# Optimization experiments

Measured on AMD Instinct MI355X. Metric: run time of the kernel, lower is better.

Reference implementation:

```python
import jax, jax.numpy as jnp
import numpy as np

LN_EPS = 1e-5


def setup_inputs() -> dict:
    key = jax.random.key(0)
    ks = jax.random.split(key, 4)
    N, D, E, Hd = 65536, 256, 8, 1024  # nodes, dim, n_experts, hidden_dim=4*dim
    s = 0.02
    return {
        "H": jax.random.normal(ks[0], (N, D), dtype=jnp.float32),
        "gate_w": jax.random.normal(ks[1], (D, E), dtype=jnp.float32) * s,
        "gate_b": jnp.zeros((E,), jnp.float32),
        "W1": jax.random.normal(ks[2], (E, D, Hd), dtype=jnp.float32) * s,
        "b1": jnp.zeros((E, Hd), jnp.float32),
        "W2": jax.random.normal(ks[3], (E, Hd, D), dtype=jnp.float32) * s,
        "b2": jnp.zeros((E, D), jnp.float32),
        "ln_gamma": jnp.ones((D,), jnp.float32),
        "ln_beta": jnp.zeros((D,), jnp.float32),
    }


def reference(H, gate_w, gate_b, W1, b1, W2, b2, ln_gamma, ln_beta):
    # Gating: softmax over experts per node. [N, E]
    weights = jax.nn.softmax(H @ gate_w + gate_b, axis=-1)
    # All experts on all nodes (dense MoE), batched over the expert axis.
    h = jax.nn.relu(jnp.einsum('nd,edh->enh', H, W1) + b1[:, None, :])   # [E, N, Hd]
    y = jnp.einsum('enh,ehd->end', h, W2) + b2[:, None, :]               # [E, N, D]
    out = jnp.einsum('ne,end->nd', weights, y)                           # gating-weighted sum
    # Residual + LayerNorm
    x = H + out
    mu = jnp.mean(x, axis=-1, keepdims=True)
    var = jnp.var(x, axis=-1, keepdims=True)
    return (x - mu) * jax.lax.rsqrt(var + LN_EPS) * ln_gamma + ln_beta
```

## Files before the change

kernel.cpp:

```cpp
#include <hip/hip_runtime.h>

#define LN_EPS 1e-5f

typedef __attribute__((ext_vector_type(8))) short bf16x8;
typedef __attribute__((ext_vector_type(4))) float f32x4;

__device__ __forceinline__ unsigned short f2bf(float f) {
    unsigned int u = __float_as_uint(f);
    u += 0x7fffu + ((u >> 16) & 1u);
    return (unsigned short)(u >> 16);
}
__device__ __forceinline__ unsigned int cvt_pk_bf16(float lo, float hi) {
    unsigned int r;
    asm("v_cvt_pk_bf16_f32 %0, %1, %2" : "=v"(r) : "v"(lo), "v"(hi));
    return r;
}

#define DD   256
#define HD   1024
#define NE   8
#define TN   64
#define LDH  264
#define GWS  260

__global__ void pack_w1(const float* __restrict__ W1, unsigned short* __restrict__ pw1) {
    int t = blockIdx.x * 256 + threadIdx.x;
    int lane = t & 63;
    int l15 = lane & 15, qd = lane >> 4;
    int tt = (t >> 6) & 31;
    int im = tt & 3, kk = tt >> 2;
    int w = (t >> 11) & 3;
    int c = (t >> 13) & 3;
    int e = t >> 15;
    int d0 = kk * 32 + qd * 8;
    int h  = c * 256 + w * 64 + im * 16 + l15;
    const float* src = W1 + ((size_t)(e * 256 + d0)) * 1024 + h;
    union { unsigned short s[8]; int4 v; } u;
#pragma unroll
    for (int j = 0; j < 8; ++j) u.s[j] = f2bf(src[(size_t)j * 1024]);
    *(int4*)(pw1 + (size_t)t * 8) = u.v;
}
__global__ void pack_w2(const float* __restrict__ W2, unsigned short* __restrict__ pw2) {
    int t = blockIdx.x * 256 + threadIdx.x;
    int lane = t & 63;
    int l15 = lane & 15, qd = lane >> 4;
    int tt = (t >> 6) & 31;
    int im = tt & 3, kk = tt >> 2;
    int w = (t >> 11) & 3;
    int c = (t >> 13) & 3;
    int e = t >> 15;
    int hd0 = c * 256 + kk * 32 + qd * 8;
    int col = w * 64 + im * 16 + l15;
    const float* src = W2 + ((size_t)(e * 1024 + hd0)) * 256 + col;
    union { unsigned short s[8]; int4 v; } u;
#pragma unroll
    for (int j = 0; j < 8; ++j) u.s[j] = f2bf(src[(size_t)j * 256]);
    *(int4*)(pw2 + (size_t)t * 8) = u.v;
}

__global__ __launch_bounds__(256, 2)
void moe_main(const float* __restrict__ H, const float* __restrict__ gate_w,
              const float* __restrict__ gate_b, const float* __restrict__ b1,
              const float* __restrict__ b2, const float* __restrict__ ln_g,
              const float* __restrict__ ln_b,
              const unsigned short* __restrict__ pw1,
              const unsigned short* __restrict__ pw2,
              float* __restrict__ out)
{
    __shared__ unsigned short sH[TN * LDH];
    __shared__ unsigned short sHC[TN * LDH];
    __shared__ float sGW[NE * GWS];
    __shared__ float sWts[NE * TN];
    __shared__ float sRed[TN * 8];
    __shared__ float sMu[TN * 2];

    const int tid  = threadIdx.x;
    const int lane = tid & 63;
    const int wave = tid >> 6;
    const int l15  = lane & 15;
    const int quad = lane >> 4;
    const int node0 = blockIdx.x * TN;
    const int ncol  = wave * 64;

    for (int i = tid; i < TN * (DD / 4); i += 256) {
        int row = i >> 6, c4 = i & 63;
        const float4 v = ((const float4*)(H + (size_t)(node0 + row) * DD))[c4];
        *(uint2*)&sH[row * LDH + c4 * 4] =
            make_uint2(cvt_pk_bf16(v.x, v.y), cvt_pk_bf16(v.z, v.w));
    }
    for (int i = tid; i < NE * DD; i += 256) {
        int e = i >> 8, d = i & 255;
        sGW[e * GWS + d] = gate_w[d * NE + e];
    }
    __syncthreads();

    bf16x8 q[4][4];
    {
        const unsigned short* p0 = pw1 + ((size_t)wave << 14) + lane * 8;
#pragma unroll
        for (int kk = 0; kk < 4; ++kk)
#pragma unroll
            for (int im = 0; im < 4; ++im)
                q[kk][im] = *(const bf16x8*)(p0 + (size_t)(kk * 4 + im) * 512);
    }

    for (int p = tid; p < TN * NE; p += 256) {
        int n = p >> 3, e = p & 7;
        const unsigned short* hr = &sH[n * LDH];
        const float* gr = &sGW[e * GWS];
        float a0 = gate_b[e], a1 = 0.f;
#pragma unroll 4
        for (int d8 = 0; d8 < 32; ++d8) {
            uint4 hv = *(const uint4*)(hr + d8 * 8);
            float4 g0 = *(const float4*)(gr + d8 * 8);
            float4 g1 = *(const float4*)(gr + d8 * 8 + 4);
            a0 = fmaf(__uint_as_float(hv.x << 16), g0.x, a0);
            a1 = fmaf(__uint_as_float(hv.x & 0xffff0000u), g0.y, a1);
            a0 = fmaf(__uint_as_float(hv.y << 16), g0.z, a0);
            a1 = fmaf(__uint_as_float(hv.y & 0xffff0000u), g0.w, a1);
            a0 = fmaf(__uint_as_float(hv.z << 16), g1.x, a0);
            a1 = fmaf(__uint_as_float(hv.z & 0xffff0000u), g1.y, a1);
            a0 = fmaf(__uint_as_float(hv.w << 16), g1.z, a0);
            a1 = fmaf(__uint_as_float(hv.w & 0xffff0000u), g1.w, a1);
        }
        sWts[e * TN + n] = a0 + a1;
    }
    __syncthreads();
    if (tid < TN) {
        float lg[8], mx = -1e30f;
#pragma unroll
        for (int e = 0; e < 8; ++e) { lg[e] = sWts[e * TN + tid]; mx = fmaxf(mx, lg[e]); }
        float ssum = 0.f;
#pragma unroll
        for (int e = 0; e < 8; ++e) { lg[e] = __expf(lg[e] - mx); ssum += lg[e]; }
        float inv = 1.0f / ssum;
#pragma unroll
        for (int e = 0; e < 8; ++e) sWts[e * TN + tid] = lg[e] * inv;
    }
    __syncthreads();

    const f32x4 ZV = {0.f, 0.f, 0.f, 0.f};
    f32x4 oacc[4][4];
#pragma unroll
    for (int i = 0; i < 4; ++i)
#pragma unroll
        for (int j = 0; j < 4; ++j) oacc[i][j] = ZV;

#pragma unroll 1
    for (int s = 0; s < 32; ++s) {
        const int e = s >> 2, c = s & 3;
        const int sn = (s + 1) & 31;

        const unsigned short* p1  = pw1 + ((size_t)(s  * 4 + wave) << 14) + lane * 8;
        const unsigned short* p2  = pw2 + ((size_t)(s  * 4 + wave) << 14) + lane * 8;
        const unsigned short* p1n = pw1 + ((size_t)(sn * 4 + wave) << 14) + lane * 8;

        f32x4 acc1[4][4];
#pragma unroll
        for (int kk = 0; kk < 8; ++kk) {
            const int slot = kk & 3;
            bf16x8 act[4], nq[4];
#pragma unroll
            for (int in = 0; in < 4; ++in)
                act[in] = *(const bf16x8*)&sH[(in * 16 + l15) * LDH + kk * 32 + quad * 8];
#pragma unroll
            for (int im = 0; im < 4; ++im)
                nq[im] = (kk < 4)
                    ? *(const bf16x8*)(p1 + (size_t)(16 + kk * 4 + im) * 512)
                    : *(const bf16x8*)(p2 + (size_t)((kk - 4) * 4 + im) * 512);
            __builtin_amdgcn_s_setprio(1);
#pragma unroll
            for (int im = 0; im < 4; ++im)
#pragma unroll
                for (int in = 0; in < 4; ++in)
                    acc1[im][in] = __builtin_amdgcn_mfma_f32_16x16x32_bf16(
                        q[slot][im], act[in], kk == 0 ? ZV : acc1[im][in], 0, 0, 0);
            __builtin_amdgcn_s_setprio(0);
#pragma unroll
            for (int im = 0; im < 4; ++im) q[slot][im] = nq[im];
        }

        float wge[4];
#pragma unroll
        for (int in = 0; in < 4; ++in) wge[in] = sWts[e * TN + in * 16 + l15];

#pragma unroll
        for (int im = 0; im < 4; ++im) {
            const float4 b1v = *(const float4*)&b1[e * HD + c * 256 + ncol + im * 16 + quad * 4];
#pragma unroll
            for (int in = 0; in < 4; ++in) {
                const float w = wge[in];
                float t0 = fmaxf(acc1[im][in][0] + b1v.x, 0.f) * w;
                float t1 = fmaxf(acc1[im][in][1] + b1v.y, 0.f) * w;
                float t2 = fmaxf(acc1[im][in][2] + b1v.z, 0.f) * w;
                float t3 = fmaxf(acc1[im][in][3] + b1v.w, 0.f) * w;
                *(uint2*)&sHC[(in * 16 + l15) * LDH + ncol + im * 16 + quad * 4] =
                    make_uint2(cvt_pk_bf16(t0, t1), cvt_pk_bf16(t2, t3));
            }
        }
        asm volatile("s_waitcnt lgkmcnt(0)" ::: "memory");
        __builtin_amdgcn_s_barrier();

#pragma unroll
        for (int kk = 0; kk < 8; ++kk) {
            const int slot = kk & 3;
            bf16x8 act[4], nq[4];
#pragma unroll
            for (int in = 0; in < 4; ++in)
                act[in] = *(const bf16x8*)&sHC[(in * 16 + l15) * LDH + kk * 32 + quad * 8];
#pragma unroll
            for (int im = 0; im < 4; ++im)
                nq[im] = (kk < 4)
                    ? *(const bf16x8*)(p2 + (size_t)(16 + kk * 4 + im) * 512)
                    : *(const bf16x8*)(p1n + (size_t)((kk - 4) * 4 + im) * 512);
            __builtin_amdgcn_s_setprio(1);
#pragma unroll
            for (int im = 0; im < 4; ++im)
#pragma unroll
                for (int in = 0; in < 4; ++in)
                    oacc[im][in] = __builtin_amdgcn_mfma_f32_16x16x32_bf16(
                        q[slot][im], act[in], oacc[im][in], 0, 0, 0);
            __builtin_amdgcn_s_setprio(0);
#pragma unroll
            for (int im = 0; im < 4; ++im) q[slot][im] = nq[im];
        }
        __builtin_amdgcn_s_barrier();
    }

    float wv[4][8];
#pragma unroll
    for (int in = 0; in < 4; ++in)
#pragma unroll
        for (int e2 = 0; e2 < 8; ++e2) wv[in][e2] = sWts[e2 * TN + in * 16 + l15];

    f32x4 wb2[4][4];
#pragma unroll
    for (int in = 0; in < 4; ++in)
#pragma unroll
        for (int im = 0; im < 4; ++im) wb2[in][im] = (f32x4){0.f, 0.f, 0.f, 0.f};
#pragma unroll
    for (int e2 = 0; e2 < 8; ++e2)
#pragma unroll
        for (int im = 0; im < 4; ++im) {
            const float4 bv = *(const float4*)&b2[e2 * DD + ncol + im * 16 + quad * 4];
#pragma unroll
            for (int in = 0; in < 4; ++in) {
                wb2[in][im][0] = fmaf(wv[in][e2], bv.x, wb2[in][im][0]);
                wb2[in][im][1] = fmaf(wv[in][e2], bv.y, wb2[in][im][1]);
                wb2[in][im][2] = fmaf(wv[in][e2], bv.z, wb2[in][im][2]);
                wb2[in][im][3] = fmaf(wv[in][e2], bv.w, wb2[in][im][3]);
            }
        }

#pragma unroll
    for (int im = 0; im < 4; ++im)
#pragma unroll
        for (int in = 0; in < 4; ++in) {
            const float4 hres = *(const float4*)
                &H[(size_t)(node0 + in * 16 + l15) * DD + ncol + im * 16 + quad * 4];
            oacc[im][in][0] += hres.x + wb2[in][im][0];
            oacc[im][in][1] += hres.y + wb2[in][im][1];
            oacc[im][in][2] += hres.z + wb2[in][im][2];
            oacc[im][in][3] += hres.w + wb2[in][im][3];
        }

    float sum[4], sum2[4];
#pragma unroll
    for (int in = 0; in < 4; ++in) {
        float s = 0.f, s2 = 0.f;
#pragma unroll
        for (int im = 0; im < 4; ++im)
#pragma unroll
            for (int r = 0; r < 4; ++r) { float x = oacc[im][in][r]; s += x; s2 += x * x; }
        s  += __shfl_xor(s, 16);  s  += __shfl_xor(s, 32);
        s2 += __shfl_xor(s2, 16); s2 += __shfl_xor(s2, 32);
        sum[in] = s; sum2[in] = s2;
    }
    if (quad == 0) {
#pragma unroll
        for (int in = 0; in < 4; ++in) {
            sRed[(in * 16 + l15) * 8 + wave * 2]     = sum[in];
            sRed[(in * 16 + l15) * 8 + wave * 2 + 1] = sum2[in];
        }
    }
    __syncthreads();
    if (tid < TN) {
        float s = 0.f, s2 = 0.f;
#pragma unroll
        for (int w2 = 0; w2 < 4; ++w2) { s += sRed[tid * 8 + w2 * 2]; s2 += sRed[tid * 8 + w2 * 2 + 1]; }
        float mu  = s * (1.0f / 256.0f);
        float var = s2 * (1.0f / 256.0f) - mu * mu;
        sMu[tid * 2] = mu;
        sMu[tid * 2 + 1] = rsqrtf(var + LN_EPS);
    }
    __syncthreads();

#pragma unroll
    for (int im = 0; im < 4; ++im) {
        const float4 lgv = *(const float4*)&ln_g[ncol + im * 16 + quad * 4];
        const float4 lbv = *(const float4*)&ln_b[ncol + im * 16 + quad * 4];
#pragma unroll
        for (int in = 0; in < 4; ++in) {
            const int node = in * 16 + l15;
            const float mu = sMu[node * 2], rs = sMu[node * 2 + 1];
            float4 y;
            y.x = (oacc[im][in][0] - mu) * rs * lgv.x + lbv.x;
            y.y = (oacc[im][in][1] - mu) * rs * lgv.y + lbv.y;
            y.z = (oacc[im][in][2] - mu) * rs * lgv.z + lbv.z;
            y.w = (oacc[im][in][3] - mu) * rs * lgv.w + lbv.w;
            *(float4*)&out[(size_t)(node0 + node) * DD + ncol + im * 16 + quad * 4] = y;
        }
    }
}

extern "C" void kernel_launch(void* const* d_in, const int* in_sizes, int n_in,
                              void* d_out, int out_size, void* d_ws, size_t ws_size,
                              hipStream_t stream) {
    const float* H   = (const float*)d_in[0];
    const float* gw  = (const float*)d_in[1];
    const float* gb  = (const float*)d_in[2];
    const float* W1  = (const float*)d_in[3];
    const float* b1  = (const float*)d_in[4];
    const float* W2  = (const float*)d_in[5];
    const float* b2  = (const float*)d_in[6];
    const float* lng = (const float*)d_in[7];
    const float* lnb = (const float*)d_in[8];
    float* out = (float*)d_out;

    unsigned short* pw1 = (unsigned short*)d_ws;
    unsigned short* pw2 = pw1 + (size_t)8 * 32 * 1024 * 8;

    hipLaunchKernelGGL(pack_w1, dim3(1024), dim3(256), 0, stream, W1, pw1);
    hipLaunchKernelGGL(pack_w2, dim3(1024), dim3(256), 0, stream, W2, pw2);
    hipLaunchKernelGGL(moe_main, dim3(65536 / TN), dim3(256), 0, stream,
                       H, gw, gb, b1, b2, lng, lnb, pw1, pw2, out);
}
```

Baseline: 583.3 us.

## Switch MoE GEMMs from 16x16x32 to 32x32x16 bf16 MFMA tiles

Replaces the 16x16x32 MFMA tiling with 32x32x16 MFMA in both expert GEMMs. The packed weight layout, accumulator fragments and epilogue indexing are rewritten to match the 32-row fragment layout. Weight prefetch now happens after each MFMA group instead of being staged in separate registers, which shortens the register live range. The larger MFMA needs fewer instructions and LDS activation reads per unit of work, but it has longer latency per instruction and makes fewer independent MFMAs available per k-step for latency hiding.

Measured after the change: 645.1 us. +10.6%, slower.

```diff
diff --git a/kernel.cpp b/kernel.cpp
--- a/kernel.cpp
+++ b/kernel.cpp
@@ -3,7 +3,7 @@
 #define LN_EPS 1e-5f
 
 typedef __attribute__((ext_vector_type(8))) short bf16x8;
-typedef __attribute__((ext_vector_type(4))) float f32x4;
+typedef __attribute__((ext_vector_type(16))) float f32x16;
 
 __device__ __forceinline__ unsigned short f2bf(float f) {
     unsigned int u = __float_as_uint(f);
@@ -26,14 +26,14 @@
 __global__ void pack_w1(const float* __restrict__ W1, unsigned short* __restrict__ pw1) {
     int t = blockIdx.x * 256 + threadIdx.x;
     int lane = t & 63;
-    int l15 = lane & 15, qd = lane >> 4;
-    int tt = (t >> 6) & 31;
-    int im = tt & 3, kk = tt >> 2;
-    int w = (t >> 11) & 3;
-    int c = (t >> 13) & 3;
-    int e = t >> 15;
-    int d0 = kk * 32 + qd * 8;
-    int h  = c * 256 + w * 64 + im * 16 + l15;
+    int l31 = lane & 31, hi = lane >> 5;
+    int f  = (t >> 6) & 1;
+    int ks = (t >> 7) & 15;
+    int w  = (t >> 11) & 3;
+    int c  = (t >> 13) & 3;
+    int e  = t >> 15;
+    int d0 = ks * 16 + hi * 8;
+    int h  = c * 256 + w * 64 + f * 32 + l31;
     const float* src = W1 + ((size_t)(e * 256 + d0)) * 1024 + h;
     union { unsigned short s[8]; int4 v; } u;
 #pragma unroll
@@ -43,14 +43,14 @@
 __global__ void pack_w2(const float* __restrict__ W2, unsigned short* __restrict__ pw2) {
     int t = blockIdx.x * 256 + threadIdx.x;
     int lane = t & 63;
-    int l15 = lane & 15, qd = lane >> 4;
-    int tt = (t >> 6) & 31;
-    int im = tt & 3, kk = tt >> 2;
-    int w = (t >> 11) & 3;
-    int c = (t >> 13) & 3;
-    int e = t >> 15;
-    int hd0 = c * 256 + kk * 32 + qd * 8;
-    int col = w * 64 + im * 16 + l15;
+    int l31 = lane & 31, hi = lane >> 5;
+    int f  = (t >> 6) & 1;
+    int ks = (t >> 7) & 15;
+    int w  = (t >> 11) & 3;
+    int c  = (t >> 13) & 3;
+    int e  = t >> 15;
+    int hd0 = c * 256 + ks * 16 + hi * 8;
+    int col = w * 64 + f * 32 + l31;
     const float* src = W2 + ((size_t)(e * 1024 + hd0)) * 256 + col;
     union { unsigned short s[8]; int4 v; } u;
 #pragma unroll
@@ -77,8 +77,8 @@
     const int tid  = threadIdx.x;
     const int lane = tid & 63;
     const int wave = tid >> 6;
-    const int l15  = lane & 15;
-    const int quad = lane >> 4;
+    const int l31  = lane & 31;
+    const int hi   = lane >> 5;
     const int node0 = blockIdx.x * TN;
     const int ncol  = wave * 64;
 
@@ -94,14 +94,14 @@
     }
     __syncthreads();
 
-    bf16x8 q[4][4];
+    bf16x8 q[4][2];
     {
         const unsigned short* p0 = pw1 + ((size_t)wave << 14) + lane * 8;
 #pragma unroll
-        for (int kk = 0; kk < 4; ++kk)
-#pragma unroll
-            for (int im = 0; im < 4; ++im)
-                q[kk][im] = *(const bf16x8*)(p0 + (size_t)(kk * 4 + im) * 512);
+        for (int ks = 0; ks < 4; ++ks)
+#pragma unroll
+            for (int f = 0; f < 2; ++f)
+                q[ks][f] = *(const bf16x8*)(p0 + (size_t)(ks * 2 + f) * 512);
     }
 
     for (int p = tid; p < TN * NE; p += 256) {
@@ -139,12 +139,12 @@
     }
     __syncthreads();
 
-    const f32x4 ZV = {0.f, 0.f, 0.f, 0.f};
-    f32x4 oacc[4][4];
-#pragma unroll
-    for (int i = 0; i < 4; ++i)
-#pragma unroll
-        for (int j = 0; j < 4; ++j) oacc[i][j] = ZV;
+    const f32x16 ZV = {0.f,0.f,0.f,0.f,0.f,0.f,0.f,0.f,0.f,0.f,0.f,0.f,0.f,0.f,0.f,0.f};
+    f32x16 oacc[2][2];
+#pragma unroll
+    for (int i = 0; i < 2; ++i)
+#pragma unroll
+        for (int j = 0; j < 2; ++j) oacc[i][j] = ZV;
 
 #pragma unroll 1
     for (int s = 0; s < 32; ++s) {
@@ -155,132 +155,139 @@
         const unsigned short* p2  = pw2 + ((size_t)(s  * 4 + wave) << 14) + lane * 8;
         const unsigned short* p1n = pw1 + ((size_t)(sn * 4 + wave) << 14) + lane * 8;
 
-        f32x4 acc1[4][4];
-#pragma unroll
-        for (int kk = 0; kk < 8; ++kk) {
-            const int slot = kk & 3;
-            bf16x8 act[4], nq[4];
-#pragma unroll
-            for (int in = 0; in < 4; ++in)
-                act[in] = *(const bf16x8*)&sH[(in * 16 + l15) * LDH + kk * 32 + quad * 8];
-#pragma unroll
-            for (int im = 0; im < 4; ++im)
-                nq[im] = (kk < 4)
-                    ? *(const bf16x8*)(p1 + (size_t)(16 + kk * 4 + im) * 512)
-                    : *(const bf16x8*)(p2 + (size_t)((kk - 4) * 4 + im) * 512);
+        f32x16 acc1[2][2];
+#pragma unroll
+        for (int ks = 0; ks < 16; ++ks) {
+            const int slot = ks & 3;
+            bf16x8 act[2];
+#pragma unroll
+            for (int fn = 0; fn < 2; ++fn)
+                act[fn] = *(const bf16x8*)&sH[(fn * 32 + l31) * LDH + ks * 16 + hi * 8];
             __builtin_amdgcn_s_setprio(1);
 #pragma unroll
-            for (int im = 0; im < 4; ++im)
-#pragma unroll
-                for (int in = 0; in < 4; ++in)
-                    acc1[im][in] = __builtin_amdgcn_mfma_f32_16x16x32_bf16(
-                        q[slot][im], act[in], kk == 0 ? ZV : acc1[im][in], 0, 0, 0);
+            for (int fh = 0; fh < 2; ++fh)
+#pragma unroll
+                for (int fn = 0; fn < 2; ++fn)
+                    acc1[fh][fn] = __builtin_amdgcn_mfma_f32_32x32x16_bf16(
+                        q[slot][fh], act[fn], ks == 0 ? ZV : acc1[fh][fn], 0, 0, 0);
             __builtin_amdgcn_s_setprio(0);
 #pragma unroll
-            for (int im = 0; im < 4; ++im) q[slot][im] = nq[im];
-        }
-
-        float wge[4];
-#pragma unroll
-        for (int in = 0; in < 4; ++in) wge[in] = sWts[e * TN + in * 16 + l15];
-
-#pragma unroll
-        for (int im = 0; im < 4; ++im) {
-            const float4 b1v = *(const float4*)&b1[e * HD + c * 256 + ncol + im * 16 + quad * 4];
-#pragma unroll
-            for (int in = 0; in < 4; ++in) {
-                const float w = wge[in];
-                float t0 = fmaxf(acc1[im][in][0] + b1v.x, 0.f) * w;
-                float t1 = fmaxf(acc1[im][in][1] + b1v.y, 0.f) * w;
-                float t2 = fmaxf(acc1[im][in][2] + b1v.z, 0.f) * w;
-                float t3 = fmaxf(acc1[im][in][3] + b1v.w, 0.f) * w;
-                *(uint2*)&sHC[(in * 16 + l15) * LDH + ncol + im * 16 + quad * 4] =
-                    make_uint2(cvt_pk_bf16(t0, t1), cvt_pk_bf16(t2, t3));
+            for (int f = 0; f < 2; ++f)
+                q[slot][f] = (ks < 12)
+                    ? *(const bf16x8*)(p1 + (size_t)((ks + 4) * 2 + f) * 512)
+                    : *(const bf16x8*)(p2 + (size_t)((ks - 12) * 2 + f) * 512);
+        }
+
+        float wge[2];
+#pragma unroll
+        for (int fn = 0; fn < 2; ++fn) wge[fn] = sWts[e * TN + fn * 32 + l31];
+
+#pragma unroll
+        for (int fh = 0; fh < 2; ++fh)
+#pragma unroll
+            for (int g = 0; g < 4; ++g) {
+                const float4 b1v = *(const float4*)
+                    &b1[e * HD + c * 256 + ncol + fh * 32 + g * 8 + hi * 4];
+#pragma unroll
+                for (int fn = 0; fn < 2; ++fn) {
+                    const float w = wge[fn];
+                    float t0 = fmaxf(acc1[fh][fn][4 * g + 0] + b1v.x, 0.f) * w;
+                    float t1 = fmaxf(acc1[fh][fn][4 * g + 1] + b1v.y, 0.f) * w;
+                    float t2 = fmaxf(acc1[fh][fn][4 * g + 2] + b1v.z, 0.f) * w;
+                    float t3 = fmaxf(acc1[fh][fn][4 * g + 3] + b1v.w, 0.f) * w;
+                    *(uint2*)&sHC[(fn * 32 + l31) * LDH + ncol + fh * 32 + g * 8 + hi * 4] =
+                        make_uint2(cvt_pk_bf16(t0, t1), cvt_pk_bf16(t2, t3));
+                }
             }
-        }
+
         asm volatile("s_waitcnt lgkmcnt(0)" ::: "memory");
         __builtin_amdgcn_s_barrier();
 
 #pragma unroll
-        for (int kk = 0; kk < 8; ++kk) {
-            const int slot = kk & 3;
-            bf16x8 act[4], nq[4];
-#pragma unroll
-            for (int in = 0; in < 4; ++in)
-                act[in] = *(const bf16x8*)&sHC[(in * 16 + l15) * LDH + kk * 32 + quad * 8];
-#pragma unroll
-            for (int im = 0; im < 4; ++im)
-                nq[im] = (kk < 4)
-                    ? *(const bf16x8*)(p2 + (size_t)(16 + kk * 4 + im) * 512)
-                    : *(const bf16x8*)(p1n + (size_t)((kk - 4) * 4 + im) * 512);
+        for (int ks = 0; ks < 16; ++ks) {
+            const int slot = ks & 3;
+            bf16x8 act[2];
+#pragma unroll
+            for (int fn = 0; fn < 2; ++fn)
+                act[fn] = *(const bf16x8*)&sHC[(fn * 32 + l31) * LDH + ks * 16 + hi * 8];
             __builtin_amdgcn_s_setprio(1);
 #pragma unroll
-            for (int im = 0; im < 4; ++im)
-#pragma unroll
-                for (int in = 0; in < 4; ++in)
-                    oacc[im][in] = __builtin_amdgcn_mfma_f32_16x16x32_bf16(
-                        q[slot][im], act[in], oacc[im][in], 0, 0, 0);
+            for (int fd = 0; fd < 2; ++fd)
+#pragma unroll
+                for (int fn = 0; fn < 2; ++fn)
+                    oacc[fd][fn] = __builtin_amdgcn_mfma_f32_32x32x16_bf16(
+                        q[slot][fd], act[fn], oacc[fd][fn], 0, 0, 0);
             __builtin_amdgcn_s_setprio(0);
 #pragma unroll
-            for (int im = 0; im < 4; ++im) q[slot][im] = nq[im];
+            for (int f = 0; f < 2; ++f)
+                q[slot][f] = (ks < 12)
+                    ? *(const bf16x8*)(p2 + (size_t)((ks + 4) * 2 + f) * 512)
+                    : *(const bf16x8*)(p1n + (size_t)((ks - 12) * 2 + f) * 512);
         }
         __builtin_amdgcn_s_barrier();
     }
 
-    float wv[4][8];
-#pragma unroll
-    for (int in = 0; in < 4; ++in)
-#pragma unroll
-        for (int e2 = 0; e2 < 8; ++e2) wv[in][e2] = sWts[e2 * TN + in * 16 + l15];
-
-    f32x4 wb2[4][4];
-#pragma unroll
-    for (int in = 0; in < 4; ++in)
-#pragma unroll
-        for (int im = 0; im < 4; ++im) wb2[in][im] = (f32x4){0.f, 0.f, 0.f, 0.f};
+    float wv[2][8];
+#pragma unroll
+    for (int fn = 0; fn < 2; ++fn)
+#pragma unroll
+        for (int e2 = 0; e2 < 8; ++e2) wv[fn][e2] = sWts[e2 * TN + fn * 32 + l31];
+
+    float4 wb2[2][2][4];
+#pragma unroll
+    for (int fn = 0; fn < 2; ++fn)
+#pragma unroll
+        for (int fd = 0; fd < 2; ++fd)
+#pragma unroll
+            for (int g = 0; g < 4; ++g) wb2[fn][fd][g] = make_float4(0.f, 0.f, 0.f, 0.f);
 #pragma unroll
     for (int e2 = 0; e2 < 8; ++e2)
 #pragma unroll
-        for (int im = 0; im < 4; ++im) {
-            const float4 bv = *(const float4*)&b2[e2 * DD + ncol + im * 16 + quad * 4];
-#pragma unroll
-            for (int in = 0; in < 4; ++in) {
-                wb2[in][im][0] = fmaf(wv[in][e2], bv.x, wb2[in][im][0]);
-                wb2[in][im][1] = fmaf(wv[in][e2], bv.y, wb2[in][im][1]);
-                wb2[in][im][2] = fmaf(wv[in][e2], bv.z, wb2[in][im][2]);
-                wb2[in][im][3] = fmaf(wv[in][e2], bv.w, wb2[in][im][3]);
+        for (int fd = 0; fd < 2; ++fd)
+#pragma unroll
+            for (int g = 0; g < 4; ++g) {
+                const float4 bv = *(const float4*)
+                    &b2[e2 * DD + ncol + fd * 32 + g * 8 + hi * 4];
+#pragma unroll
+                for (int fn = 0; fn < 2; ++fn) {
+                    wb2[fn][fd][g].x = fmaf(wv[fn][e2], bv.x, wb2[fn][fd][g].x);
+                    wb2[fn][fd][g].y = fmaf(wv[fn][e2], bv.y, wb2[fn][fd][g].y);
+                    wb2[fn][fd][g].z = fmaf(wv[fn][e2], bv.z, wb2[fn][fd][g].z);
+                    wb2[fn][fd][g].w = fmaf(wv[fn][e2], bv.w, wb2[fn][fd][g].w);
+                }
             }
-        }
-
-#pragma unroll
-    for (int im = 0; im < 4; ++im)
-#pragma unroll
-        for (int in = 0; in < 4; ++in) {
-            const float4 hres = *(const float4*)
-                &H[(size_t)(node0 + in * 16 + l15) * DD + ncol + im * 16 + quad * 4];
-            oacc[im][in][0] += hres.x + wb2[in][im][0];
-            oacc[im][in][1] += hres.y + wb2[in][im][1];
-            oacc[im][in][2] += hres.z + wb2[in][im][2];
-            oacc[im][in][3] += hres.w + wb2[in][im][3];
-        }
-
-    float sum[4], sum2[4];
-#pragma unroll
-    for (int in = 0; in < 4; ++in) {
+
+#pragma unroll
+    for (int fd = 0; fd < 2; ++fd)
+#pragma unroll
+        for (int fn = 0; fn < 2; ++fn)
+#pragma unroll
+            for (int g = 0; g < 4; ++g) {
+                const float4 hres = *(const float4*)
+                    &H[(size_t)(node0 + fn * 32 + l31) * DD + ncol + fd * 32 + g * 8 + hi * 4];
+                oacc[fd][fn][4 * g + 0] += hres.x + wb2[fn][fd][g].x;
+                oacc[fd][fn][4 * g + 1] += hres.y + wb2[fn][fd][g].y;
+                oacc[fd][fn][4 * g + 2] += hres.z + wb2[fn][fd][g].z;
+                oacc[fd][fn][4 * g + 3] += hres.w + wb2[fn][fd][g].w;
+            }
+
+    float sum[2], sum2[2];
+#pragma unroll
+    for (int fn = 0; fn < 2; ++fn) {
         float s = 0.f, s2 = 0.f;
 #pragma unroll
-        for (int im = 0; im < 4; ++im)
-#pragma unroll
-            for (int r = 0; r < 4; ++r) { float x = oacc[im][in][r]; s += x; s2 += x * x; }
-        s  += __shfl_xor(s, 16);  s  += __shfl_xor(s, 32);
-        s2 += __shfl_xor(s2, 16); s2 += __shfl_xor(s2, 32);
-        sum[in] = s; sum2[in] = s2;
-    }
-    if (quad == 0) {
-#pragma unroll
-        for (int in = 0; in < 4; ++in) {
-            sRed[(in * 16 + l15) * 8 + wave * 2]     = sum[in];
-            sRed[(in * 16 + l15) * 8 + wave * 2 + 1] = sum2[in];
+        for (int fd = 0; fd < 2; ++fd)
+#pragma unroll
+            for (int r = 0; r < 16; ++r) { float x = oacc[fd][fn][r]; s += x; s2 += x * x; }
+        s  += __shfl_xor(s, 32);
+        s2 += __shfl_xor(s2, 32);
+        sum[fn] = s; sum2[fn] = s2;
+    }
+    if (hi == 0) {
+#pragma unroll
+        for (int fn = 0; fn < 2; ++fn) {
+            sRed[(fn * 32 + l31) * 8 + wave * 2]     = sum[fn];
+            sRed[(fn * 32 + l31) * 8 + wave * 2 + 1] = sum2[fn];
         }
     }
     __syncthreads();
@@ -296,21 +303,23 @@
     __syncthreads();
 
 #pragma unroll
-    for (int im = 0; im < 4; ++im) {
-        const float4 lgv = *(const float4*)&ln_g[ncol + im * 16 + quad * 4];
-        const float4 lbv = *(const float4*)&ln_b[ncol + im * 16 + quad * 4];
-#pragma unroll
-        for (int in = 0; in < 4; ++in) {
-            const int node = in * 16 + l15;
-            const float mu = sMu[node * 2], rs = sMu[node * 2 + 1];
-            float4 y;
-            y.x = (oacc[im][in][0] - mu) * rs * lgv.x + lbv.x;
-            y.y = (oacc[im][in][1] - mu) * rs * lgv.y + lbv.y;
-            y.z = (oacc[im][in][2] - mu) * rs * lgv.z + lbv.z;
-            y.w = (oacc[im][in][3] - mu) * rs * lgv.w + lbv.w;
-            *(float4*)&out[(size_t)(node0 + node) * DD + ncol + im * 16 + quad * 4] = y;
-        }
-    }
+    for (int fd = 0; fd < 2; ++fd)
+#pragma unroll
+        for (int g = 0; g < 4; ++g) {
+            const float4 lgv = *(const float4*)&ln_g[ncol + fd * 32 + g * 8 + hi * 4];
+            const float4 lbv = *(const float4*)&ln_b[ncol + fd * 32 + g * 8 + hi * 4];
+#pragma unroll
+            for (int fn = 0; fn < 2; ++fn) {
+                const int node = fn * 32 + l31;
+                const float mu = sMu[node * 2], rs = sMu[node * 2 + 1];
+                float4 y;
+                y.x = (oacc[fd][fn][4 * g + 0] - mu) * rs * lgv.x + lbv.x;
+                y.y = (oacc[fd][fn][4 * g + 1] - mu) * rs * lgv.y + lbv.y;
+                y.z = (oacc[fd][fn][4 * g + 2] - mu) * rs * lgv.z + lbv.z;
+                y.w = (oacc[fd][fn][4 * g + 3] - mu) * rs * lgv.w + lbv.w;
+                *(float4*)&out[(size_t)(node0 + node) * DD + ncol + fd * 32 + g * 8 + hi * 4] = y;
+            }
+        }
 }
 
 extern "C" void kernel_launch(void* const* d_in, const int* in_sizes, int n_in,
```

## Split each node tile across eight waves with half-width weight fragments

Applied to the files above, without the earlier changes.

Doubles the block to 512 threads (8 waves). Each wave now owns 32 output columns instead of 64, which halves the per-wave accumulator and prefetched-weight register arrays. The weight packing kernels are re-laid out to match, sRed is aliased onto sGW to save LDS, and the launch bounds target 4 blocks per CU for higher occupancy. In exchange, every wave still reads the full activation tile from LDS, so LDS read traffic per MFMA doubles, and extra barriers are added.

Result: slower. 885.1 us (+51.7%).

```diff
diff --git a/kernel.cpp b/kernel.cpp
--- a/kernel.cpp
+++ b/kernel.cpp
@@ -22,18 +22,19 @@
 #define TN   64
 #define LDH  264
 #define GWS  260
+#define NW   8
 
 __global__ void pack_w1(const float* __restrict__ W1, unsigned short* __restrict__ pw1) {
     int t = blockIdx.x * 256 + threadIdx.x;
     int lane = t & 63;
     int l15 = lane & 15, qd = lane >> 4;
-    int tt = (t >> 6) & 31;
-    int im = tt & 3, kk = tt >> 2;
-    int w = (t >> 11) & 3;
+    int fr = (t >> 6) & 15;
+    int im = fr & 1, kk = fr >> 1;
+    int w = (t >> 10) & 7;
     int c = (t >> 13) & 3;
     int e = t >> 15;
     int d0 = kk * 32 + qd * 8;
-    int h  = c * 256 + w * 64 + im * 16 + l15;
+    int h  = c * 256 + w * 32 + im * 16 + l15;
     const float* src = W1 + ((size_t)(e * 256 + d0)) * 1024 + h;
     union { unsigned short s[8]; int4 v; } u;
 #pragma unroll
@@ -44,13 +45,13 @@
     int t = blockIdx.x * 256 + threadIdx.x;
     int lane = t & 63;
     int l15 = lane & 15, qd = lane >> 4;
-    int tt = (t >> 6) & 31;
-    int im = tt & 3, kk = tt >> 2;
-    int w = (t >> 11) & 3;
+    int fr = (t >> 6) & 15;
+    int im = fr & 1, kk = fr >> 1;
+    int w = (t >> 10) & 7;
     int c = (t >> 13) & 3;
     int e = t >> 15;
     int hd0 = c * 256 + kk * 32 + qd * 8;
-    int col = w * 64 + im * 16 + l15;
+    int col = w * 32 + im * 16 + l15;
     const float* src = W2 + ((size_t)(e * 1024 + hd0)) * 256 + col;
     union { unsigned short s[8]; int4 v; } u;
 #pragma unroll
@@ -58,7 +59,7 @@
     *(int4*)(pw2 + (size_t)t * 8) = u.v;
 }
 
-__global__ __launch_bounds__(256, 2)
+__global__ __launch_bounds__(512, 4)
 void moe_main(const float* __restrict__ H, const float* __restrict__ gate_w,
               const float* __restrict__ gate_b, const float* __restrict__ b1,
               const float* __restrict__ b2, const float* __restrict__ ln_g,
@@ -71,8 +72,9 @@
     __shared__ unsigned short sHC[TN * LDH];
     __shared__ float sGW[NE * GWS];
     __shared__ float sWts[NE * TN];
-    __shared__ float sRed[TN * 8];
     __shared__ float sMu[TN * 2];
+
+    float* const sRed = sGW;
 
     const int tid  = threadIdx.x;
     const int lane = tid & 63;
@@ -80,31 +82,33 @@
     const int l15  = lane & 15;
     const int quad = lane >> 4;
     const int node0 = blockIdx.x * TN;
-    const int ncol  = wave * 64;
-
-    for (int i = tid; i < TN * (DD / 4); i += 256) {
+    const int ncol  = wave * 32;
+    const int loff  = lane * 8;
+
+    for (int i = tid; i < TN * (DD / 4); i += 512) {
         int row = i >> 6, c4 = i & 63;
         const float4 v = ((const float4*)(H + (size_t)(node0 + row) * DD))[c4];
         *(uint2*)&sH[row * LDH + c4 * 4] =
             make_uint2(cvt_pk_bf16(v.x, v.y), cvt_pk_bf16(v.z, v.w));
     }
-    for (int i = tid; i < NE * DD; i += 256) {
+    for (int i = tid; i < NE * DD; i += 512) {
         int e = i >> 8, d = i & 255;
         sGW[e * GWS + d] = gate_w[d * NE + e];
     }
     __syncthreads();
 
-    bf16x8 q[4][4];
+    bf16x8 q[4][2];
     {
-        const unsigned short* p0 = pw1 + ((size_t)wave << 14) + lane * 8;
+        const unsigned short* p0 = pw1 + ((size_t)wave << 13);
 #pragma unroll
         for (int kk = 0; kk < 4; ++kk)
 #pragma unroll
-            for (int im = 0; im < 4; ++im)
-                q[kk][im] = *(const bf16x8*)(p0 + (size_t)(kk * 4 + im) * 512);
-    }
-
-    for (int p = tid; p < TN * NE; p += 256) {
+            for (int im = 0; im < 2; ++im)
+                q[kk][im] = *(const bf16x8*)(p0 + (size_t)(kk * 2 + im) * 512 + loff);
+    }
+
+    {
+        int p = tid;
         int n = p >> 3, e = p & 7;
         const unsigned short* hr = &sH[n * LDH];
         const float* gr = &sGW[e * GWS];
@@ -123,6 +127,7 @@
             a0 = fmaf(__uint_as_float(hv.w << 16), g1.z, a0);
             a1 = fmaf(__uint_as_float(hv.w & 0xffff0000u), g1.w, a1);
         }
+        __syncthreads();
         sWts[e * TN + n] = a0 + a1;
     }
     __syncthreads();
@@ -140,9 +145,9 @@
     __syncthreads();
 
     const f32x4 ZV = {0.f, 0.f, 0.f, 0.f};
-    f32x4 oacc[4][4];
-#pragma unroll
-    for (int i = 0; i < 4; ++i)
+    f32x4 oacc[2][4];
+#pragma unroll
+    for (int i = 0; i < 2; ++i)
 #pragma unroll
         for (int j = 0; j < 4; ++j) oacc[i][j] = ZV;
 
@@ -151,33 +156,33 @@
         const int e = s >> 2, c = s & 3;
         const int sn = (s + 1) & 31;
 
-        const unsigned short* p1  = pw1 + ((size_t)(s  * 4 + wave) << 14) + lane * 8;
-        const unsigned short* p2  = pw2 + ((size_t)(s  * 4 + wave) << 14) + lane * 8;
-        const unsigned short* p1n = pw1 + ((size_t)(sn * 4 + wave) << 14) + lane * 8;
-
-        f32x4 acc1[4][4];
+        const unsigned short* p1  = pw1 + ((size_t)(s  * NW + wave) << 13);
+        const unsigned short* p2  = pw2 + ((size_t)(s  * NW + wave) << 13);
+        const unsigned short* p1n = pw1 + ((size_t)(sn * NW + wave) << 13);
+
+        f32x4 acc1[2][4];
 #pragma unroll
         for (int kk = 0; kk < 8; ++kk) {
             const int slot = kk & 3;
-            bf16x8 act[4], nq[4];
+            bf16x8 act[4], nq[2];
 #pragma unroll
             for (int in = 0; in < 4; ++in)
                 act[in] = *(const bf16x8*)&sH[(in * 16 + l15) * LDH + kk * 32 + quad * 8];
 #pragma unroll
-            for (int im = 0; im < 4; ++im)
+            for (int im = 0; im < 2; ++im)
                 nq[im] = (kk < 4)
-                    ? *(const bf16x8*)(p1 + (size_t)(16 + kk * 4 + im) * 512)
-                    : *(const bf16x8*)(p2 + (size_t)((kk - 4) * 4 + im) * 512);
+                    ? *(const bf16x8*)(p1 + (size_t)((kk + 4) * 2 + im) * 512 + loff)
+                    : *(const bf16x8*)(p2 + (size_t)((kk - 4) * 2 + im) * 512 + loff);
             __builtin_amdgcn_s_setprio(1);
 #pragma unroll
-            for (int im = 0; im < 4; ++im)
+            for (int im = 0; im < 2; ++im)
 #pragma unroll
                 for (int in = 0; in < 4; ++in)
                     acc1[im][in] = __builtin_amdgcn_mfma_f32_16x16x32_bf16(
                         q[slot][im], act[in], kk == 0 ? ZV : acc1[im][in], 0, 0, 0);
             __builtin_amdgcn_s_setprio(0);
 #pragma unroll
-            for (int im = 0; im < 4; ++im) q[slot][im] = nq[im];
+            for (int im = 0; im < 2; ++im) q[slot][im] = nq[im];
         }
 
         float wge[4];
@@ -185,7 +190,7 @@
         for (int in = 0; in < 4; ++in) wge[in] = sWts[e * TN + in * 16 + l15];
 
 #pragma unroll
-        for (int im = 0; im < 4; ++im) {
+        for (int im = 0; im < 2; ++im) {
             const float4 b1v = *(const float4*)&b1[e * HD + c * 256 + ncol + im * 16 + quad * 4];
 #pragma unroll
             for (int in = 0; in < 4; ++in) {
@@ -204,25 +209,25 @@
 #pragma unroll
         for (int kk = 0; kk < 8; ++kk) {
             const int slot = kk & 3;
-            bf16x8 act[4], nq[4];
+            bf16x8 act[4], nq[2];
 #pragma unroll
             for (int in = 0; in < 4; ++in)
                 act[in] = *(const bf16x8*)&sHC[(in * 16 + l15) * LDH + kk * 32 + quad * 8];
 #pragma unroll
-            for (int im = 0; im < 4; ++im)
+            for (int im = 0; im < 2; ++im)
                 nq[im] = (kk < 4)
-                    ? *(const bf16x8*)(p2 + (size_t)(16 + kk * 4 + im) * 512)
-                    : *(const bf16x8*)(p1n + (size_t)((kk - 4) * 4 + im) * 512);
+                    ? *(const bf16x8*)(p2 + (size_t)((kk + 4) * 2 + im) * 512 + loff)
+                    : *(const bf16x8*)(p1n + (size_t)((kk - 4) * 2 + im) * 512 + loff);
             __builtin_amdgcn_s_setprio(1);
 #pragma unroll
-            for (int im = 0; im < 4; ++im)
+            for (int im = 0; im < 2; ++im)
 #pragma unroll
                 for (int in = 0; in < 4; ++in)
                     oacc[im][in] = __builtin_amdgcn_mfma_f32_16x16x32_bf16(
                         q[slot][im], act[in], oacc[im][in], 0, 0, 0);
             __builtin_amdgcn_s_setprio(0);
 #pragma unroll
-            for (int im = 0; im < 4; ++im) q[slot][im] = nq[im];
+            for (int im = 0; im < 2; ++im) q[slot][im] = nq[im];
         }
         __builtin_amdgcn_s_barrier();
     }
@@ -233,15 +238,15 @@
 #pragma unroll
         for (int e2 = 0; e2 < 8; ++e2) wv[in][e2] = sWts[e2 * TN + in * 16 + l15];
 
-    f32x4 wb2[4][4];
+    f32x4 wb2[4][2];
 #pragma unroll
     for (int in = 0; in < 4; ++in)
 #pragma unroll
-        for (int im = 0; im < 4; ++im) wb2[in][im] = (f32x4){0.f, 0.f, 0.f, 0.f};
+        for (int im = 0; im < 2; ++im) wb2[in][im] = (f32x4){0.f, 0.f, 0.f, 0.f};
 #pragma unroll
     for (int e2 = 0; e2 < 8; ++e2)
 #pragma unroll
-        for (int im = 0; im < 4; ++im) {
+        for (int im = 0; im < 2; ++im) {
             const float4 bv = *(const float4*)&b2[e2 * DD + ncol + im * 16 + quad * 4];
 #pragma unroll
             for (int in = 0; in < 4; ++in) {
@@ -253,7 +258,7 @@
         }
 
 #pragma unroll
-    for (int im = 0; im < 4; ++im)
+    for (int im = 0; im < 2; ++im)
 #pragma unroll
         for (int in = 0; in < 4; ++in) {
             const float4 hres = *(const float4*)
@@ -269,25 +274,29 @@
     for (int in = 0; in < 4; ++in) {
         float s = 0.f, s2 = 0.f;
 #pragma unroll
-        for (int im = 0; im < 4; ++im)
+        for (int im = 0; im < 2; ++im)
 #pragma unroll
             for (int r = 0; r < 4; ++r) { float x = oacc[im][in][r]; s += x; s2 += x * x; }
         s  += __shfl_xor(s, 16);  s  += __shfl_xor(s, 32);
         s2 += __shfl_xor(s2, 16); s2 += __shfl_xor(s2, 32);
         sum[in] = s; sum2[in] = s2;
     }
+    __syncthreads();
     if (quad == 0) {
 #pragma unroll
         for (int in = 0; in < 4; ++in) {
-            sRed[(in * 16 + l15) * 8 + wave * 2]     = sum[in];
-            sRed[(in * 16 + l15) * 8 + wave * 2 + 1] = sum2[in];
+            sRed[(in * 16 + l15) * 16 + wave * 2]     = sum[in];
+            sRed[(in * 16 + l15) * 16 + wave * 2 + 1] = sum2[in];
         }
     }
     __syncthreads();
     if (tid < TN) {
         float s = 0.f, s2 = 0.f;
 #pragma unroll
-        for (int w2 = 0; w2 < 4; ++w2) { s += sRed[tid * 8 + w2 * 2]; s2 += sRed[tid * 8 + w2 * 2 + 1]; }
+        for (int w2 = 0; w2 < NW; ++w2) {
+            s  += sRed[tid * 16 + w2 * 2];
+            s2 += sRed[tid * 16 + w2 * 2 + 1];
+        }
         float mu  = s * (1.0f / 256.0f);
         float var = s2 * (1.0f / 256.0f) - mu * mu;
         sMu[tid * 2] = mu;
@@ -296,7 +305,7 @@
     __syncthreads();
 
 #pragma unroll
-    for (int im = 0; im < 4; ++im) {
+    for (int im = 0; im < 2; ++im) {
         const float4 lgv = *(const float4*)&ln_g[ncol + im * 16 + quad * 4];
         const float4 lbv = *(const float4*)&ln_b[ncol + im * 16 + quad * 4];
 #pragma unroll
@@ -332,6 +341,6 @@
 
     hipLaunchKernelGGL(pack_w1, dim3(1024), dim3(256), 0, stream, W1, pw1);
     hipLaunchKernelGGL(pack_w2, dim3(1024), dim3(256), 0, stream, W2, pw2);
-    hipLaunchKernelGGL(moe_main, dim3(65536 / TN), dim3(256), 0, stream,
+    hipLaunchKernelGGL(moe_main, dim3(65536 / TN), dim3(512), 0, stream,
                        H, gw, gb, b1, b2, lng, lnb, pw1, pw2, out);
 }
```

## Split node tile across two wave groups with 512-thread blocks

Applied to the files above, without the earlier changes.

Doubles the block to 8 waves, with each group of 4 waves handling 32 of the 64 nodes, so each wave keeps half the accumulators and activation fragments. The weight prefetch ring shrinks from four slots to two, and sRed now aliases the gate-weight shared buffer to save LDS. The aim is lower register pressure and more resident waves (waves_per_eu 4) to hide latency. The cost is that every weight fragment is now loaded twice per block, once by each node group, which doubles weight traffic from global/L2. The shallower prefetch may also expose load latency.

Measured after the change: 895.2 us. 1.53x slower.

```diff
diff --git a/kernel.cpp b/kernel.cpp
--- a/kernel.cpp
+++ b/kernel.cpp
@@ -22,6 +22,7 @@
 #define TN   64
 #define LDH  264
 #define GWS  260
+#define NW   8
 
 __global__ void pack_w1(const float* __restrict__ W1, unsigned short* __restrict__ pw1) {
     int t = blockIdx.x * 256 + threadIdx.x;
@@ -58,7 +59,7 @@
     *(int4*)(pw2 + (size_t)t * 8) = u.v;
 }
 
-__global__ __launch_bounds__(256, 2)
+__global__ __launch_bounds__(512) __attribute__((amdgpu_waves_per_eu(4)))
 void moe_main(const float* __restrict__ H, const float* __restrict__ gate_w,
               const float* __restrict__ gate_b, const float* __restrict__ b1,
               const float* __restrict__ b2, const float* __restrict__ ln_g,
@@ -71,41 +72,46 @@
     __shared__ unsigned short sHC[TN * LDH];
     __shared__ float sGW[NE * GWS];
     __shared__ float sWts[NE * TN];
-    __shared__ float sRed[TN * 8];
     __shared__ float sMu[TN * 2];
+
+    float* const sRed = sGW;
 
     const int tid  = threadIdx.x;
     const int lane = tid & 63;
     const int wave = tid >> 6;
+    const int wc   = wave & 3;
+    const int ng   = wave >> 2;
     const int l15  = lane & 15;
     const int quad = lane >> 4;
     const int node0 = blockIdx.x * TN;
-    const int ncol  = wave * 64;
-
-    for (int i = tid; i < TN * (DD / 4); i += 256) {
+    const int ncol  = wc * 64;
+    const int nrow  = ng * 32;
+    const int loff  = lane * 8;
+
+    for (int i = tid; i < TN * (DD / 4); i += 512) {
         int row = i >> 6, c4 = i & 63;
         const float4 v = ((const float4*)(H + (size_t)(node0 + row) * DD))[c4];
         *(uint2*)&sH[row * LDH + c4 * 4] =
             make_uint2(cvt_pk_bf16(v.x, v.y), cvt_pk_bf16(v.z, v.w));
     }
-    for (int i = tid; i < NE * DD; i += 256) {
+    for (int i = tid; i < NE * DD; i += 512) {
         int e = i >> 8, d = i & 255;
         sGW[e * GWS + d] = gate_w[d * NE + e];
     }
     __syncthreads();
 
-    bf16x8 q[4][4];
+    bf16x8 q[2][4];
     {
-        const unsigned short* p0 = pw1 + ((size_t)wave << 14) + lane * 8;
-#pragma unroll
-        for (int kk = 0; kk < 4; ++kk)
-#pragma unroll
-            for (int im = 0; im < 4; ++im)
-                q[kk][im] = *(const bf16x8*)(p0 + (size_t)(kk * 4 + im) * 512);
-    }
-
-    for (int p = tid; p < TN * NE; p += 256) {
-        int n = p >> 3, e = p & 7;
+        const unsigned short* p0 = pw1 + ((size_t)wc << 14);
+#pragma unroll
+        for (int kk = 0; kk < 2; ++kk)
+#pragma unroll
+            for (int im = 0; im < 4; ++im)
+                q[kk][im] = *(const bf16x8*)(p0 + (size_t)(kk * 4 + im) * 512 + loff);
+    }
+
+    {
+        int n = tid >> 3, e = tid & 7;
         const unsigned short* hr = &sH[n * LDH];
         const float* gr = &sGW[e * GWS];
         float a0 = gate_b[e], a1 = 0.f;
@@ -140,61 +146,59 @@
     __syncthreads();
 
     const f32x4 ZV = {0.f, 0.f, 0.f, 0.f};
-    f32x4 oacc[4][4];
+    f32x4 oacc[4][2];
 #pragma unroll
     for (int i = 0; i < 4; ++i)
 #pragma unroll
-        for (int j = 0; j < 4; ++j) oacc[i][j] = ZV;
+        for (int j = 0; j < 2; ++j) oacc[i][j] = ZV;
 
 #pragma unroll 1
     for (int s = 0; s < 32; ++s) {
         const int e = s >> 2, c = s & 3;
         const int sn = (s + 1) & 31;
 
-        const unsigned short* p1  = pw1 + ((size_t)(s  * 4 + wave) << 14) + lane * 8;
-        const unsigned short* p2  = pw2 + ((size_t)(s  * 4 + wave) << 14) + lane * 8;
-        const unsigned short* p1n = pw1 + ((size_t)(sn * 4 + wave) << 14) + lane * 8;
-
-        f32x4 acc1[4][4];
+        const unsigned short* p1  = pw1 + ((size_t)(s  * 4 + wc) << 14);
+        const unsigned short* p2  = pw2 + ((size_t)(s  * 4 + wc) << 14);
+        const unsigned short* p1n = pw1 + ((size_t)(sn * 4 + wc) << 14);
+
+        f32x4 acc1[4][2];
 #pragma unroll
         for (int kk = 0; kk < 8; ++kk) {
-            const int slot = kk & 3;
-            bf16x8 act[4], nq[4];
-#pragma unroll
-            for (int in = 0; in < 4; ++in)
-                act[in] = *(const bf16x8*)&sH[(in * 16 + l15) * LDH + kk * 32 + quad * 8];
-#pragma unroll
-            for (int im = 0; im < 4; ++im)
-                nq[im] = (kk < 4)
-                    ? *(const bf16x8*)(p1 + (size_t)(16 + kk * 4 + im) * 512)
-                    : *(const bf16x8*)(p2 + (size_t)((kk - 4) * 4 + im) * 512);
+            const int slot = kk & 1;
+            bf16x8 act[2];
+#pragma unroll
+            for (int in = 0; in < 2; ++in)
+                act[in] = *(const bf16x8*)&sH[(nrow + in * 16 + l15) * LDH + kk * 32 + quad * 8];
             __builtin_amdgcn_s_setprio(1);
 #pragma unroll
             for (int im = 0; im < 4; ++im)
 #pragma unroll
-                for (int in = 0; in < 4; ++in)
+                for (int in = 0; in < 2; ++in)
                     acc1[im][in] = __builtin_amdgcn_mfma_f32_16x16x32_bf16(
                         q[slot][im], act[in], kk == 0 ? ZV : acc1[im][in], 0, 0, 0);
             __builtin_amdgcn_s_setprio(0);
 #pragma unroll
-            for (int im = 0; im < 4; ++im) q[slot][im] = nq[im];
-        }
-
-        float wge[4];
-#pragma unroll
-        for (int in = 0; in < 4; ++in) wge[in] = sWts[e * TN + in * 16 + l15];
+            for (int im = 0; im < 4; ++im)
+                q[slot][im] = (kk < 6)
+                    ? *(const bf16x8*)(p1 + (size_t)((kk + 2) * 4 + im) * 512 + loff)
+                    : *(const bf16x8*)(p2 + (size_t)((kk - 6) * 4 + im) * 512 + loff);
+        }
+
+        float wge[2];
+#pragma unroll
+        for (int in = 0; in < 2; ++in) wge[in] = sWts[e * TN + nrow + in * 16 + l15];
 
 #pragma unroll
         for (int im = 0; im < 4; ++im) {
             const float4 b1v = *(const float4*)&b1[e * HD + c * 256 + ncol + im * 16 + quad * 4];
 #pragma unroll
-            for (int in = 0; in < 4; ++in) {
+            for (int in = 0; in < 2; ++in) {
                 const float w = wge[in];
                 float t0 = fmaxf(acc1[im][in][0] + b1v.x, 0.f) * w;
                 float t1 = fmaxf(acc1[im][in][1] + b1v.y, 0.f) * w;
                 float t2 = fmaxf(acc1[im][in][2] + b1v.z, 0.f) * w;
                 float t3 = fmaxf(acc1[im][in][3] + b1v.w, 0.f) * w;
-                *(uint2*)&sHC[(in * 16 + l15) * LDH + ncol + im * 16 + quad * 4] =
+                *(uint2*)&sHC[(nrow + in * 16 + l15) * LDH + ncol + im * 16 + quad * 4] =
                     make_uint2(cvt_pk_bf16(t0, t1), cvt_pk_bf16(t2, t3));
             }
         }
@@ -203,39 +207,37 @@
 
 #pragma unroll
         for (int kk = 0; kk < 8; ++kk) {
-            const int slot = kk & 3;
-            bf16x8 act[4], nq[4];
-#pragma unroll
-            for (int in = 0; in < 4; ++in)
-                act[in] = *(const bf16x8*)&sHC[(in * 16 + l15) * LDH + kk * 32 + quad * 8];
-#pragma unroll
-            for (int im = 0; im < 4; ++im)
-                nq[im] = (kk < 4)
-                    ? *(const bf16x8*)(p2 + (size_t)(16 + kk * 4 + im) * 512)
-                    : *(const bf16x8*)(p1n + (size_t)((kk - 4) * 4 + im) * 512);
+            const int slot = kk & 1;
+            bf16x8 act[2];
+#pragma unroll
+            for (int in = 0; in < 2; ++in)
+                act[in] = *(const bf16x8*)&sHC[(nrow + in * 16 + l15) * LDH + kk * 32 + quad * 8];
             __builtin_amdgcn_s_setprio(1);
 #pragma unroll
             for (int im = 0; im < 4; ++im)
 #pragma unroll
-                for (int in = 0; in < 4; ++in)
+                for (int in = 0; in < 2; ++in)
                     oacc[im][in] = __builtin_amdgcn_mfma_f32_16x16x32_bf16(
                         q[slot][im], act[in], oacc[im][in], 0, 0, 0);
             __builtin_amdgcn_s_setprio(0);
 #pragma unroll
-            for (int im = 0; im < 4; ++im) q[slot][im] = nq[im];
+            for (int im = 0; im < 4; ++im)
+                q[slot][im] = (kk < 6)
+                    ? *(const bf16x8*)(p2 + (size_t)((kk + 2) * 4 + im) * 512 + loff)
+                    : *(const bf16x8*)(p1n + (size_t)((kk - 6) * 4 + im) * 512 + loff);
         }
         __builtin_amdgcn_s_barrier();
     }
 
-    float wv[4][8];
-#pragma unroll
-    for (int in = 0; in < 4; ++in)
-#pragma unroll
-        for (int e2 = 0; e2 < 8; ++e2) wv[in][e2] = sWts[e2 * TN + in * 16 + l15];
-
-    f32x4 wb2[4][4];
-#pragma unroll
-    for (int in = 0; in < 4; ++in)
+    float wv[2][8];
+#pragma unroll
+    for (int in = 0; in < 2; ++in)
+#pragma unroll
+        for (int e2 = 0; e2 < 8; ++e2) wv[in][e2] = sWts[e2 * TN + nrow + in * 16 + l15];
+
+    f32x4 wb2[2][4];
+#pragma unroll
+    for (int in = 0; in < 2; ++in)
 #pragma unroll
         for (int im = 0; im < 4; ++im) wb2[in][im] = (f32x4){0.f, 0.f, 0.f, 0.f};
 #pragma unroll
@@ -244,7 +246,7 @@
         for (int im = 0; im < 4; ++im) {
             const float4 bv = *(const float4*)&b2[e2 * DD + ncol + im * 16 + quad * 4];
 #pragma unroll
-            for (int in = 0; in < 4; ++in) {
+            for (int in = 0; in < 2; ++in) {
                 wb2[in][im][0] = fmaf(wv[in][e2], bv.x, wb2[in][im][0]);
                 wb2[in][im][1] = fmaf(wv[in][e2], bv.y, wb2[in][im][1]);
                 wb2[in][im][2] = fmaf(wv[in][e2], bv.z, wb2[in][im][2]);
@@ -255,18 +257,18 @@
 #pragma unroll
     for (int im = 0; im < 4; ++im)
 #pragma unroll
-        for (int in = 0; in < 4; ++in) {
+        for (int in = 0; in < 2; ++in) {
             const float4 hres = *(const float4*)
-                &H[(size_t)(node0 + in * 16 + l15) * DD + ncol + im * 16 + quad * 4];
+                &H[(size_t)(node0 + nrow + in * 16 + l15) * DD + ncol + im * 16 + quad * 4];
             oacc[im][in][0] += hres.x + wb2[in][im][0];
             oacc[im][in][1] += hres.y + wb2[in][im][1];
             oacc[im][in][2] += hres.z + wb2[in][im][2];
             oacc[im][in][3] += hres.w + wb2[in][im][3];
         }
 
-    float sum[4], sum2[4];
-#pragma unroll
-    for (int in = 0; in < 4; ++in) {
+    float sum[2], sum2[2];
+#pragma unroll
+    for (int in = 0; in < 2; ++in) {
         float s = 0.f, s2 = 0.f;
 #pragma unroll
         for (int im = 0; im < 4; ++im)
@@ -276,18 +278,22 @@
         s2 += __shfl_xor(s2, 16); s2 += __shfl_xor(s2, 32);
         sum[in] = s; sum2[in] = s2;
     }
+    __syncthreads();
     if (quad == 0) {
 #pragma unroll
-        for (int in = 0; in < 4; ++in) {
-            sRed[(in * 16 + l15) * 8 + wave * 2]     = sum[in];
-            sRed[(in * 16 + l15) * 8 + wave * 2 + 1] = sum2[in];
+        for (int in = 0; in < 2; ++in) {
+            sRed[(nrow + in * 16 + l15) * 8 + wc * 2]     = sum[in];
+            sRed[(nrow + in * 16 + l15) * 8 + wc * 2 + 1] = sum2[in];
         }
     }
     __syncthreads();
     if (tid < TN) {
         float s = 0.f, s2 = 0.f;
 #pragma unroll
-        for (int w2 = 0; w2 < 4; ++w2) { s += sRed[tid * 8 + w2 * 2]; s2 += sRed[tid * 8 + w2 * 2 + 1]; }
+        for (int w2 = 0; w2 < 4; ++w2) {
+            s  += sRed[tid * 8 + w2 * 2];
+            s2 += sRed[tid * 8 + w2 * 2 + 1];
+        }
         float mu  = s * (1.0f / 256.0f);
         float var = s2 * (1.0f / 256.0f) - mu * mu;
         sMu[tid * 2] = mu;
@@ -300,8 +306,8 @@
         const float4 lgv = *(const float4*)&ln_g[ncol + im * 16 + quad * 4];
         const float4 lbv = *(const float4*)&ln_b[ncol + im * 16 + quad * 4];
 #pragma unroll
-        for (int in = 0; in < 4; ++in) {
-            const int node = in * 16 + l15;
+        for (int in = 0; in < 2; ++in) {
+            const int node = nrow + in * 16 + l15;
             const float mu = sMu[node * 2], rs = sMu[node * 2 + 1];
             float4 y;
             y.x = (oacc[im][in][0] - mu) * rs * lgv.x + lbv.x;
@@ -332,6 +338,6 @@
 
     hipLaunchKernelGGL(pack_w1, dim3(1024), dim3(256), 0, stream, W1, pw1);
     hipLaunchKernelGGL(pack_w2, dim3(1024), dim3(256), 0, stream, W2, pw2);
-    hipLaunchKernelGGL(moe_main, dim3(65536 / TN), dim3(256), 0, stream,
+    hipLaunchKernelGGL(moe_main, dim3(65536 / TN), dim3(512), 0, stream,
                        H, gw, gb, b1, b2, lng, lnb, pw1, pw2, out);
 }
```
